# Kernel tuning notes

Measured on AMD Instinct MI355X. Metric: run time of the kernel, lower is better.

Reference implementation:

```python
import jax, jax.numpy as jnp
import numpy as np

B, S, D = 4, 4096, 64
TEMPERATURE = 8.0  # sqrt(64), matching Dense(64) projections in source


def setup_inputs() -> dict:
    key = jax.random.key(0)
    kq, kk, kv = jax.random.split(key, 3)
    q = jax.random.normal(kq, (B, S, D), dtype=jnp.float32)
    k = jax.random.normal(kk, (B, S, D), dtype=jnp.float32)
    v = jax.random.normal(kv, (B, S, D), dtype=jnp.float32)
    return {"q": q, "k": k, "v": v}


def reference(q, k, v):
    # attn = softmax(QK^T / temperature); dropout is identity at inference
    scores = jnp.einsum("bqd,bkd->bqk", q, k) / TEMPERATURE  # [B,S,S]
    attn = jax.nn.softmax(scores, axis=-1)
    out = jnp.einsum("bqk,bkd->bqd", attn, v)  # [B,S,D]
    return (out, attn)
```

## Files before the change

kernel.cpp:

```cpp
#include <hip/hip_runtime.h>
#include <cstddef>

namespace {
constexpr int kB = 4;
constexpr int kS = 4096;
constexpr int kD = 64;
constexpr float kC = 0.18033688011112042f;

typedef float  f32x4  __attribute__((ext_vector_type(4)));
typedef __bf16 bf16x8 __attribute__((ext_vector_type(8)));
typedef short  s16x2  __attribute__((ext_vector_type(2)));
typedef short  s16x4  __attribute__((ext_vector_type(4)));
typedef short  s16x8  __attribute__((ext_vector_type(8)));
typedef int    i32x4  __attribute__((ext_vector_type(4)));

constexpr size_t kWsQ = (size_t)kB * kS * kD;
constexpr size_t kWsNeed = 3 * kWsQ * sizeof(short);
}

__device__ __forceinline__ s16x2 pack_bf16(float a, float b) {
    __bf16 ha = (__bf16)a, hb = (__bf16)b;
    s16x2 r;
    r.x = __builtin_bit_cast(short, ha);
    r.y = __builtin_bit_cast(short, hb);
    return r;
}

__global__ __launch_bounds__(256)
void prepass_kernel(const float* __restrict__ q, const float* __restrict__ k,
                    const float* __restrict__ v, short* __restrict__ qb,
                    short* __restrict__ kb, short* __restrict__ vt)
{
    __shared__ float lt[64][65];
    const int bid = blockIdx.x, tid = threadIdx.x;
    if (bid < 512) {
        const float* src = (bid < 256) ? q : k;
        short* dst = (bid < 256) ? qb : kb;
        const int base = (bid & 255) * 4096;
        #pragma unroll
        for (int c = 0; c < 4; ++c) {
            const int idx = base + c * 1024 + tid * 4;
            float4 f = *(const float4*)(src + idx);
            s16x4 o = __builtin_shufflevector(pack_bf16(f.x, f.y), pack_bf16(f.z, f.w), 0, 1, 2, 3);
            *(s16x4*)(dst + idx) = o;
        }
    } else {
        const int vb = bid - 512;
        const int b = vb >> 6, j0 = (vb & 63) * 64;
        const int r = tid >> 2, seg = tid & 3;
        const float* vrow = v + ((size_t)(b * kS) + j0 + r) * kD + seg * 16;
        #pragma unroll
        for (int u = 0; u < 4; ++u) {
            float4 f = *(const float4*)(vrow + 4 * u);
            lt[r][seg * 16 + 4 * u + 0] = f.x;
            lt[r][seg * 16 + 4 * u + 1] = f.y;
            lt[r][seg * 16 + 4 * u + 2] = f.z;
            lt[r][seg * 16 + 4 * u + 3] = f.w;
        }
        __syncthreads();
        const int d = r, js = seg * 16;
        short* drow = vt + ((size_t)(b * kD) + d) * kS + j0 + js;
        #pragma unroll
        for (int w = 0; w < 4; ++w) {
            s16x4 o = __builtin_shufflevector(
                pack_bf16(lt[js + 4 * w + 0][d], lt[js + 4 * w + 1][d]),
                pack_bf16(lt[js + 4 * w + 2][d], lt[js + 4 * w + 3][d]), 0, 1, 2, 3);
            *(s16x4*)(drow + 4 * w) = o;
        }
    }
}

__global__ __launch_bounds__(512, 8)
void attn_mfma_kernel(const short* __restrict__ qb, const short* __restrict__ kb,
                      const short* __restrict__ vt, float* __restrict__ outg,
                      float* __restrict__ attng)
{
    __shared__ __align__(16) float lds_pool[8 * 16 * 68];
    __shared__ float lds_rs[8][16];
    __shared__ float lds_linv[16];

    const int swz = (blockIdx.x & 7) * 128 + (blockIdx.x >> 3);
    const int b  = swz >> 8;
    const int i0 = (swz & 255) * 16;
    const int lane = threadIdx.x & 63;
    const int wave = threadIdx.x >> 6;
    const int t = lane & 15;
    const int q = lane >> 4;

    const short* Qb = qb + ((size_t)(b * kS) + i0) * kD;
    const short* Kb = kb + (size_t)(b * kS) * kD;
    const short* Vt = vt + (size_t)b * kD * kS;

    const bf16x8 qf0 = *(const bf16x8*)(Qb + t * kD + 8 * q);
    const bf16x8 qf1 = *(const bf16x8*)(Qb + t * kD + 32 + 8 * q);

    const int jbeg = wave * (kS / 8);
    const int jend = jbeg + (kS / 8);
    const int sA = t + 32 * (q & 1);

    f32x4 oacc[4];
    #pragma unroll
    for (int dt = 0; dt < 4; ++dt) oacc[dt] = (f32x4){0.f, 0.f, 0.f, 0.f};
    float rs = 0.f;

    for (int j0 = jbeg; j0 < jend; j0 += 32) {
        int p0 = 0, p1 = 0, p2 = 0, p3 = 0;
        #pragma unroll
        for (int h = 0; h < 2; ++h) {
            const short* p = Kb + (size_t)(j0 + 16 * h + t) * kD + 8 * q;
            const bf16x8 ka0 = *(const bf16x8*)p;
            const bf16x8 ka1 = *(const bf16x8*)(p + 32);
            f32x4 acc = (f32x4){0.f, 0.f, 0.f, 0.f};
            acc = __builtin_amdgcn_mfma_f32_16x16x32_bf16(ka0, qf0, acc, 0, 0, 0);
            acc = __builtin_amdgcn_mfma_f32_16x16x32_bf16(ka1, qf1, acc, 0, 0, 0);
            const float e0 = __builtin_amdgcn_exp2f(acc[0] * kC);
            const float e1 = __builtin_amdgcn_exp2f(acc[1] * kC);
            const float e2 = __builtin_amdgcn_exp2f(acc[2] * kC);
            const float e3 = __builtin_amdgcn_exp2f(acc[3] * kC);
            rs += (e0 + e1) + (e2 + e3);
            const int d0 = __builtin_bit_cast(int, pack_bf16(e0, e1));
            const int d1 = __builtin_bit_cast(int, pack_bf16(e2, e3));
            const int a0 = __shfl(d0, sA);
            const int a1 = __shfl(d1, sA);
            const int b0 = __shfl(d0, sA + 16);
            const int b1 = __shfl(d1, sA + 16);
            if ((q >> 1) == h) { p0 = a0; p1 = a1; p2 = b0; p3 = b1; }
        }
        const i32x4 pi = (i32x4){p0, p1, p2, p3};
        const bf16x8 pa = __builtin_bit_cast(bf16x8, pi);

        #pragma unroll
        for (int dt = 0; dt < 4; ++dt) {
            const bf16x8 vb = *(const bf16x8*)(Vt + (size_t)(16 * dt + t) * kS + j0 + 8 * q);
            oacc[dt] = __builtin_amdgcn_mfma_f32_16x16x32_bf16(pa, vb, oacc[dt], 0, 0, 0);
        }
    }

    rs += __shfl_xor(rs, 16);
    rs += __shfl_xor(rs, 32);

    if (lane < 16) lds_rs[wave][t] = rs;
    if (wave > 0) {
        #pragma unroll
        for (int dt = 0; dt < 4; ++dt)
            #pragma unroll
            for (int r = 0; r < 4; ++r)
                lds_pool[((wave - 1) * 16 + 4 * q + r) * 68 + 16 * dt + t] = oacc[dt][r];
    }
    __syncthreads();
    if (wave == 0) {
        #pragma unroll
        for (int w = 0; w < 7; ++w)
            #pragma unroll
            for (int dt = 0; dt < 4; ++dt)
                #pragma unroll
                for (int r = 0; r < 4; ++r)
                    oacc[dt][r] += lds_pool[(w * 16 + 4 * q + r) * 68 + 16 * dt + t];
        float tot = 0.f;
        #pragma unroll
        for (int w = 0; w < 8; ++w) tot += lds_rs[w][t];
        if (lane < 16) lds_linv[t] = 1.0f / tot;
    }
    __syncthreads();

    if (wave == 0) {
        #pragma unroll
        for (int r = 0; r < 4; ++r) {
            const float li = lds_linv[4 * q + r];
            float* orow = outg + ((size_t)(b * kS) + i0 + 4 * q + r) * kD + t;
            #pragma unroll
            for (int dt = 0; dt < 4; ++dt)
                orow[16 * dt] = oacc[dt][r] * li;
        }
    }
    const float li_t = lds_linv[t];

    float* stw = lds_pool + wave * (16 * 68);
    const int srow = lane >> 4;
    const int scol = (lane & 15) * 4;
    float* abase0 = attng + ((size_t)(b * kS) + i0 + 0 + srow) * kS + scol;
    float* abase1 = attng + ((size_t)(b * kS) + i0 + 4 + srow) * kS + scol;
    float* abase2 = attng + ((size_t)(b * kS) + i0 + 8 + srow) * kS + scol;
    float* abase3 = attng + ((size_t)(b * kS) + i0 + 12 + srow) * kS + scol;

    for (int jb = jbeg; jb < jend; jb += 64) {
        #pragma unroll
        for (int m = 0; m < 4; ++m) {
            const int j0 = jb + 16 * m;
            const short* p = Kb + (size_t)(j0 + t) * kD + 8 * q;
            const bf16x8 ka0 = *(const bf16x8*)p;
            const bf16x8 ka1 = *(const bf16x8*)(p + 32);
            f32x4 acc = (f32x4){0.f, 0.f, 0.f, 0.f};
            acc = __builtin_amdgcn_mfma_f32_16x16x32_bf16(ka0, qf0, acc, 0, 0, 0);
            acc = __builtin_amdgcn_mfma_f32_16x16x32_bf16(ka1, qf1, acc, 0, 0, 0);
            f32x4 o;
            o[0] = __builtin_amdgcn_exp2f(acc[0] * kC) * li_t;
            o[1] = __builtin_amdgcn_exp2f(acc[1] * kC) * li_t;
            o[2] = __builtin_amdgcn_exp2f(acc[2] * kC) * li_t;
            o[3] = __builtin_amdgcn_exp2f(acc[3] * kC) * li_t;
            *(f32x4*)&stw[t * 68 + 16 * m + 4 * q] = o;
        }
        #pragma unroll
        for (int s = 0; s < 4; ++s) {
            const int row = 4 * s + srow;
            const f32x4 vld = *(const f32x4*)&stw[row * 68 + scol];
            float* dst = (s == 0 ? abase0 : s == 1 ? abase1 : s == 2 ? abase2 : abase3) + jb;
            __builtin_nontemporal_store(vld, (f32x4*)dst);
        }
    }
}

namespace fb {
constexpr int QT = 64, JT = 64;
constexpr float kScale = 0.125f;
constexpr int LP = kD + 4;
}
__global__ __launch_bounds__(256, 1)
void attn_fp32_kernel(const float* __restrict__ qg, const float* __restrict__ kg,
                      const float* __restrict__ vg, float* __restrict__ outg,
                      float* __restrict__ attng)
{
    using namespace fb;
    __shared__ float qs[QT][LP];
    __shared__ float ks[JT][LP];
    __shared__ float es[QT][JT + 4];
    __shared__ float red[QT][17];
    __shared__ float linv[QT];
    const int tid = threadIdx.x;
    const int tx = tid & 15, ty = tid >> 4;
    const int b = blockIdx.x >> 6, qt = blockIdx.x & 63, i0 = qt * QT;
    const float* qbp = qg + ((size_t)b * kS + i0) * kD;
    const float* kbase = kg + (size_t)b * kS * kD;
    const float* vbase = vg + (size_t)b * kS * kD;
    {
        const int r = tid >> 4, c4 = (tid & 15) * 4;
        #pragma unroll
        for (int m = 0; m < 4; ++m)
            *(float4*)&qs[r + 16 * m][c4] = *(const float4*)(qbp + (r + 16 * m) * kD + c4);
    }
    float oacc[4][4]; float rsv[4];
    #pragma unroll
    for (int r = 0; r < 4; ++r) { rsv[r] = 0.f; for (int c = 0; c < 4; ++c) oacc[r][c] = 0.f; }
    for (int jt = 0; jt < kS / JT; ++jt) {
        const float* kt = kbase + (size_t)(jt * JT) * kD;
        const int r = tid >> 4, c4 = (tid & 15) * 4;
        #pragma unroll
        for (int m = 0; m < 4; ++m)
            *(float4*)&ks[r + 16 * m][c4] = *(const float4*)(kt + (r + 16 * m) * kD + c4);
        __syncthreads();
        float acc[4][4] = {{0.f}};
        #pragma unroll
        for (int d4 = 0; d4 < kD / 4; ++d4) {
            float4 qa[4], kav[4];
            #pragma unroll
            for (int r2 = 0; r2 < 4; ++r2) qa[r2] = *(const float4*)&qs[ty * 4 + r2][d4 * 4];
            #pragma unroll
            for (int c = 0; c < 4; ++c) kav[c] = *(const float4*)&ks[tx * 4 + c][d4 * 4];
            #pragma unroll
            for (int r2 = 0; r2 < 4; ++r2)
                #pragma unroll
                for (int c = 0; c < 4; ++c)
                    acc[r2][c] += qa[r2].x * kav[c].x + qa[r2].y * kav[c].y
                                + qa[r2].z * kav[c].z + qa[r2].w * kav[c].w;
        }
        #pragma unroll
        for (int r2 = 0; r2 < 4; ++r2) {
            float4 e4;
            e4.x = __expf(acc[r2][0] * kScale); e4.y = __expf(acc[r2][1] * kScale);
            e4.z = __expf(acc[r2][2] * kScale); e4.w = __expf(acc[r2][3] * kScale);
            rsv[r2] += (e4.x + e4.y) + (e4.z + e4.w);
            *(float4*)&es[ty * 4 + r2][tx * 4] = e4;
        }
        __syncthreads();
        const float* vt2 = vbase + (size_t)(jt * JT) * kD;
        #pragma unroll 4
        for (int j4 = 0; j4 < JT / 4; ++j4) {
            float4 vv[4], ea[4];
            #pragma unroll
            for (int n = 0; n < 4; ++n) vv[n] = *(const float4*)(vt2 + (size_t)(j4 * 4 + n) * kD + tx * 4);
            #pragma unroll
            for (int r2 = 0; r2 < 4; ++r2) ea[r2] = *(const float4*)&es[ty * 4 + r2][j4 * 4];
            #pragma unroll
            for (int r2 = 0; r2 < 4; ++r2) {
                oacc[r2][0] += ea[r2].x * vv[0].x + ea[r2].y * vv[1].x + ea[r2].z * vv[2].x + ea[r2].w * vv[3].x;
                oacc[r2][1] += ea[r2].x * vv[0].y + ea[r2].y * vv[1].y + ea[r2].z * vv[2].y + ea[r2].w * vv[3].y;
                oacc[r2][2] += ea[r2].x * vv[0].z + ea[r2].y * vv[1].z + ea[r2].z * vv[2].z + ea[r2].w * vv[3].z;
                oacc[r2][3] += ea[r2].x * vv[0].w + ea[r2].y * vv[1].w + ea[r2].z * vv[2].w + ea[r2].w * vv[3].w;
            }
        }
        __syncthreads();
    }
    #pragma unroll
    for (int r = 0; r < 4; ++r) red[ty * 4 + r][tx] = rsv[r];
    __syncthreads();
    if (tid < QT) {
        float s = 0.f;
        #pragma unroll
        for (int t2 = 0; t2 < 16; ++t2) s += red[tid][t2];
        linv[tid] = 1.0f / s;
    }
    __syncthreads();
    {
        float* ob = outg + ((size_t)b * kS + i0) * kD;
        #pragma unroll
        for (int r = 0; r < 4; ++r) {
            const int i = ty * 4 + r; const float li = linv[i];
            float4 o4; o4.x = oacc[r][0] * li; o4.y = oacc[r][1] * li;
            o4.z = oacc[r][2] * li; o4.w = oacc[r][3] * li;
            *(float4*)(ob + (size_t)i * kD + tx * 4) = o4;
        }
    }
    float* ab = attng + ((size_t)b * kS + i0) * kS;
    for (int jt = 0; jt < kS / JT; ++jt) {
        const float* kt = kbase + (size_t)(jt * JT) * kD;
        const int r = tid >> 4, c4 = (tid & 15) * 4;
        #pragma unroll
        for (int m = 0; m < 4; ++m)
            *(float4*)&ks[r + 16 * m][c4] = *(const float4*)(kt + (r + 16 * m) * kD + c4);
        __syncthreads();
        float acc[4][4] = {{0.f}};
        #pragma unroll
        for (int d4 = 0; d4 < kD / 4; ++d4) {
            float4 qa[4], kav[4];
            #pragma unroll
            for (int r2 = 0; r2 < 4; ++r2) qa[r2] = *(const float4*)&qs[ty * 4 + r2][d4 * 4];
            #pragma unroll
            for (int c = 0; c < 4; ++c) kav[c] = *(const float4*)&ks[tx * 4 + c][d4 * 4];
            #pragma unroll
            for (int r2 = 0; r2 < 4; ++r2)
                #pragma unroll
                for (int c = 0; c < 4; ++c)
                    acc[r2][c] += qa[r2].x * kav[c].x + qa[r2].y * kav[c].y
                                + qa[r2].z * kav[c].z + qa[r2].w * kav[c].w;
        }
        #pragma unroll
        for (int r2 = 0; r2 < 4; ++r2) {
            const int i = ty * 4 + r2; const float li = linv[i];
            float4 e4;
            e4.x = __expf(acc[r2][0] * kScale) * li; e4.y = __expf(acc[r2][1] * kScale) * li;
            e4.z = __expf(acc[r2][2] * kScale) * li; e4.w = __expf(acc[r2][3] * kScale) * li;
            *(float4*)(ab + (size_t)i * kS + jt * JT + tx * 4) = e4;
        }
        __syncthreads();
    }
}

extern "C" void kernel_launch(void* const* d_in, const int* in_sizes, int n_in,
                              void* d_out, int out_size, void* d_ws, size_t ws_size,
                              hipStream_t stream) {
    const float* q = (const float*)d_in[0];
    const float* k = (const float*)d_in[1];
    const float* v = (const float*)d_in[2];
    float* out  = (float*)d_out;
    float* attn = out + (size_t)kB * kS * kD;

    if (ws_size >= kWsNeed) {
        short* qb = (short*)d_ws;
        short* kbp = qb + kWsQ;
        short* vt = kbp + kWsQ;
        prepass_kernel<<<dim3(768), 256, 0, stream>>>(q, k, v, qb, kbp, vt);
        attn_mfma_kernel<<<dim3(kB * (kS / 16)), 512, 0, stream>>>(qb, kbp, vt, out, attn);
    } else {
        attn_fp32_kernel<<<dim3(kB * (kS / 64)), 256, 0, stream>>>(q, k, v, out, attn);
    }
}
```

Baseline: 423.6 us.

## Split attention into separate PV/normalizer kernel and attn-store kernel

Splits the fused attention kernel into two launches. The first computes the PV product and the per-row inverse softmax denominators and writes those to workspace. The second recomputes QK^T and writes the normalized attention matrix. This decouples the compute-heavy phase from the store-bound phase so each kernel can run with simpler register and LDS usage, at the cost of recomputing the scores and an extra launch.

```diff
diff --git a/kernel.cpp b/kernel.cpp
--- a/kernel.cpp
+++ b/kernel.cpp
@@ -15,7 +15,8 @@
 typedef int    i32x4  __attribute__((ext_vector_type(4)));
 
 constexpr size_t kWsQ = (size_t)kB * kS * kD;
-constexpr size_t kWsNeed = 3 * kWsQ * sizeof(short);
+constexpr size_t kWsLinv = (size_t)kB * kS;
+constexpr size_t kWsNeed = 3 * kWsQ * sizeof(short) + kWsLinv * sizeof(float);
 }
 
 __device__ __forceinline__ s16x2 pack_bf16(float a, float b) {
@@ -71,11 +72,11 @@
 }
 
 __global__ __launch_bounds__(512, 8)
-void attn_mfma_kernel(const short* __restrict__ qb, const short* __restrict__ kb,
-                      const short* __restrict__ vt, float* __restrict__ outg,
-                      float* __restrict__ attng)
+void attn_pv_kernel(const short* __restrict__ qb, const short* __restrict__ kb,
+                    const short* __restrict__ vt, float* __restrict__ outg,
+                    float* __restrict__ linv_ws)
 {
-    __shared__ __align__(16) float lds_pool[8 * 16 * 68];
+    __shared__ __align__(16) float lds_out[7][16][68];
     __shared__ float lds_rs[8][16];
     __shared__ float lds_linv[16];
 
@@ -145,7 +146,7 @@
         for (int dt = 0; dt < 4; ++dt)
             #pragma unroll
             for (int r = 0; r < 4; ++r)
-                lds_pool[((wave - 1) * 16 + 4 * q + r) * 68 + 16 * dt + t] = oacc[dt][r];
+                lds_out[wave - 1][4 * q + r][16 * dt + t] = oacc[dt][r];
     }
     __syncthreads();
     if (wave == 0) {
@@ -155,11 +156,15 @@
             for (int dt = 0; dt < 4; ++dt)
                 #pragma unroll
                 for (int r = 0; r < 4; ++r)
-                    oacc[dt][r] += lds_pool[(w * 16 + 4 * q + r) * 68 + 16 * dt + t];
+                    oacc[dt][r] += lds_out[w][4 * q + r][16 * dt + t];
         float tot = 0.f;
         #pragma unroll
         for (int w = 0; w < 8; ++w) tot += lds_rs[w][t];
-        if (lane < 16) lds_linv[t] = 1.0f / tot;
+        if (lane < 16) {
+            const float li = 1.0f / tot;
+            lds_linv[t] = li;
+            linv_ws[(size_t)(b * kS) + i0 + t] = li;
+        }
     }
     __syncthreads();
 
@@ -173,9 +178,34 @@
                 orow[16 * dt] = oacc[dt][r] * li;
         }
     }
-    const float li_t = lds_linv[t];
-
-    float* stw = lds_pool + wave * (16 * 68);
+}
+
+__global__ __launch_bounds__(512, 8)
+void attn_store_kernel(const short* __restrict__ qb, const short* __restrict__ kb,
+                       const float* __restrict__ linv_ws, float* __restrict__ attng)
+{
+    __shared__ __align__(16) float stg[8][16][68];
+
+    const int swz = (blockIdx.x & 7) * 128 + (blockIdx.x >> 3);
+    const int b  = swz >> 8;
+    const int i0 = (swz & 255) * 16;
+    const int lane = threadIdx.x & 63;
+    const int wave = threadIdx.x >> 6;
+    const int t = lane & 15;
+    const int q = lane >> 4;
+
+    const short* Qb = qb + ((size_t)(b * kS) + i0) * kD;
+    const short* Kb = kb + (size_t)(b * kS) * kD;
+
+    const bf16x8 qf0 = *(const bf16x8*)(Qb + t * kD + 8 * q);
+    const bf16x8 qf1 = *(const bf16x8*)(Qb + t * kD + 32 + 8 * q);
+
+    const int jbeg = wave * (kS / 8);
+    const int jend = jbeg + (kS / 8);
+
+    const float li_t = linv_ws[(size_t)(b * kS) + i0 + t];
+
+    float* stw = &stg[wave][0][0];
     const int srow = lane >> 4;
     const int scol = (lane & 15) * 4;
     float* abase0 = attng + ((size_t)(b * kS) + i0 + 0 + srow) * kS + scol;
@@ -358,8 +388,10 @@
         short* qb = (short*)d_ws;
         short* kbp = qb + kWsQ;
         short* vt = kbp + kWsQ;
+        float* linv_ws = (float*)(vt + kWsQ);
         prepass_kernel<<<dim3(768), 256, 0, stream>>>(q, k, v, qb, kbp, vt);
-        attn_mfma_kernel<<<dim3(kB * (kS / 16)), 512, 0, stream>>>(qb, kbp, vt, out, attn);
+        attn_pv_kernel<<<dim3(kB * (kS / 16)), 512, 0, stream>>>(qb, kbp, vt, out, linv_ws);
+        attn_store_kernel<<<dim3(kB * (kS / 16)), 512, 0, stream>>>(qb, kbp, linv_ws, attn);
     } else {
         attn_fp32_kernel<<<dim3(kB * (kS / 64)), 256, 0, stream>>>(q, k, v, out, attn);
     }
```

Measured after the change: 423.4 us. Within noise of the previous version (-0.0%).
